# Performance work log

Hardware: AMD Instinct MI355X
Metric: run time of the kernel (lower is better)

The kernel has to match this reference:

```python
import jax, jax.numpy as jnp
import numpy as np
from jax import lax

B, S, H = 2, 512, 2048          # batch, seq, hidden_size
I = 768                          # moe_intermediate_size
E = 64                           # num_experts
K = 8                            # num_experts_per_tok (top_k)


def setup_inputs() -> dict:
    key = jax.random.key(0)
    k1, k2, k3, k4 = jax.random.split(key, 4)
    hidden_states = jax.random.normal(k1, (B, S, H), jnp.float32)
    gate_weight = jax.random.normal(k2, (E, H), jnp.float32) * 0.02
    gate_up_weights = jax.random.normal(k3, (E, H, 2 * I), jnp.float32) * 0.02
    down_weights = jax.random.normal(k4, (E, I, H), jnp.float32) * 0.02
    return {
        "hidden_states": hidden_states,
        "gate_weight": gate_weight,
        "gate_up_weights": gate_up_weights,
        "down_weights": down_weights,
    }


def reference(hidden_states, gate_weight, gate_up_weights, down_weights):
    orig_shape = hidden_states.shape
    x = hidden_states.reshape(-1, H)          # [T, H]
    T = x.shape[0]

    # Router: softmax in fp32, top-k, renormalize (norm_topk_prob=True)
    logits = x @ gate_weight.T                # [T, E]
    probs = jax.nn.softmax(logits.astype(jnp.float32), axis=-1)
    routing_weights, selected_experts = lax.top_k(probs, K)   # [T, K]
    wsum = routing_weights.sum(axis=-1, keepdims=True)
    wsum = jnp.where(wsum == 0, 1.0, wsum)
    routing_weights = (routing_weights / wsum).astype(x.dtype)

    # Dense combine matrix [T, E]: zero weight for unselected experts.
    combine = jnp.zeros((T, E), x.dtype).at[
        jnp.arange(T)[:, None], selected_experts
    ].add(routing_weights)

    # Scan over experts; each step is one batched GEMM over all tokens,
    # masked/weighted by the combine weights (same math as per-token loop).
    def body(acc, ws):
        wgu, wd, we = ws                      # [H,2I], [I,H], [T]
        gu = x @ wgu                          # [T, 2I]
        gate, up = jnp.split(gu, 2, axis=-1)  # [T, I] each
        act = jax.nn.silu(gate) * up          # SwiGLU
        out = act @ wd                        # [T, H]
        return acc + we[:, None] * out, None

    init = jnp.zeros_like(x)
    final, _ = lax.scan(body, init, (gate_up_weights, down_weights, combine.T))
    return final.reshape(orig_shape)
```

## Files before the change

kernel.cpp:

```cpp
#include <hip/hip_runtime.h>
#include <hip/hip_bf16.h>
#include <hip/hip_fp16.h>

typedef unsigned int uint32;
typedef unsigned short u16;

#define TOK 1024
#define HID 2048
#define NEXP 64
#define TOPK 8
#define IMED 768
#define IMED2 1536

typedef __attribute__((ext_vector_type(8))) _Float16 half8;
typedef __attribute__((ext_vector_type(4))) float f32x4;

static __device__ __forceinline__ uint32 pack2(float a, float b) {
  union { _Float16 h[2]; uint32 u; } p;
  p.h[0] = (_Float16)a; p.h[1] = (_Float16)b;
  return p.u;
}
static __device__ __forceinline__ u16 f2h(float a) {
  union { _Float16 h; u16 u; } p;
  p.h = (_Float16)a;
  return p.u;
}

__global__ __launch_bounds__(256) void router_kernel(
    const float* __restrict__ x, const float* __restrict__ gw,
    int* __restrict__ topk_id, float* __restrict__ topk_w,
    u16* __restrict__ xh) {
  int t0 = blockIdx.x << 2;
  __shared__ float part[4][NEXP][5];
  int tid = threadIdx.x;
  int e = tid & 63, p = tid >> 6;
  const float* gwp = gw + (size_t)e * HID + (p << 9);
  const float* xp = x + (size_t)t0 * HID + (p << 9);
  float acc[4] = {0.f, 0.f, 0.f, 0.f};
  for (int i = 0; i < 128; i++) {
    float4 w = ((const float4*)gwp)[i];
    #pragma unroll
    for (int t = 0; t < 4; t++) {
      float4 xv = *(const float4*)(xp + (size_t)t * HID + (i << 2));
      acc[t] += w.x * xv.x + w.y * xv.y + w.z * xv.z + w.w * xv.w;
    }
  }
  #pragma unroll
  for (int t = 0; t < 4; t++) part[p][e][t] = acc[t];
  for (int i = tid; i < 2048; i += 256) {
    int r = i >> 9;
    int c = i & 511;
    float4 v = *(const float4*)(x + (size_t)(t0 + r) * HID + (c << 2));
    uint2 hp;
    hp.x = pack2(v.x, v.y);
    hp.y = pack2(v.z, v.w);
    *(uint2*)(xh + (size_t)(t0 + r) * HID + (c << 2)) = hp;
  }
  __syncthreads();
  int wv = tid >> 6, l = tid & 63;
  int t = t0 + wv;
  float lg = part[0][l][wv] + part[1][l][wv] + part[2][l][wv] + part[3][l][wv];
  float m = lg;
  #pragma unroll
  for (int d = 1; d < 64; d <<= 1) m = fmaxf(m, __shfl_xor(m, d));
  float v = __expf(lg - m);
  float w8[TOPK]; int i8[TOPK]; float wsum = 0.f;
  #pragma unroll
  for (int k = 0; k < TOPK; k++) {
    float bv = v; int bi = l;
    #pragma unroll
    for (int d = 1; d < 64; d <<= 1) {
      float ov = __shfl_xor(bv, d);
      int oi = __shfl_xor(bi, d);
      if (ov > bv || (ov == bv && oi < bi)) { bv = ov; bi = oi; }
    }
    w8[k] = bv; i8[k] = bi; wsum += bv;
    if (l == bi) v = -1.f;
  }
  if (l == 0) {
    float rinv = 1.f / wsum;
    #pragma unroll
    for (int k = 0; k < TOPK; k++) {
      topk_id[t * TOPK + k] = i8[k];
      topk_w[t * TOPK + k] = w8[k] * rinv;
    }
  }
}

__global__ __launch_bounds__(256) void scatter_kernel(
    const int* __restrict__ topk_id, const float* __restrict__ topk_w,
    int* __restrict__ off, int* __restrict__ gcnt,
    int* __restrict__ row_tok, float* __restrict__ row_w,
    int* __restrict__ inv) {
  int e = blockIdx.x;
  __shared__ int lcnt[NEXP];
  __shared__ int sbase;
  __shared__ int scur;
  int tid = threadIdx.x;
  if (tid < NEXP) lcnt[tid] = 0;
  __syncthreads();
  for (int i = tid; i < TOK * TOPK; i += 256) atomicAdd(&lcnt[topk_id[i]], 1);
  __syncthreads();
  if (tid < 64) {
    int c = lcnt[tid];
    int xv = c;
    #pragma unroll
    for (int d = 1; d < 64; d <<= 1) {
      int y = __shfl_up(xv, d);
      if (tid >= d) xv += y;
    }
    if (tid == e) {
      sbase = xv - c;
      off[e] = xv - c;
      gcnt[e] = c;
    }
    if (tid == 0) scur = 0;
  }
  __syncthreads();
  int base = sbase;
  for (int i = tid; i < TOK * TOPK; i += 256) {
    if (topk_id[i] == e) {
      int p = atomicAdd(&scur, 1);
      row_tok[base + p] = i >> 3;
      row_w[base + p] = topk_w[i];
      inv[i] = base + p;
    }
  }
}

__global__ __launch_bounds__(512, 2) void gateup_kernel(
    const u16* __restrict__ xh, const float* __restrict__ Wgu,
    const int* __restrict__ off, const int* __restrict__ cnt,
    const int* __restrict__ row_tok, u16* __restrict__ act) {
  int bid = blockIdx.x;
  int xcd = bid & 7, s2 = bid >> 3;
  int e = xcd + ((s2 & 7) << 3);
  int slab = s2 >> 3;
  int r0 = off[e];
  int ne = cnt[e];
  int c0 = slab * 96;

  __shared__ __align__(16) char AsB[256 * 80];
  __shared__ __align__(16) char BsB[192 * 80];

  int tid = threadIdx.x;
  int lane = tid & 63;
  int wid = tid >> 6;
  int wm = wid >> 1, wn = wid & 1;
  int fr = lane & 15, hi = lane >> 4;

  int arow = tid >> 1, aseg = tid & 1;
  int tok = row_tok[r0 + ((arow < ne) ? arow : 0)];
  const u16* xa = xh + (size_t)tok * HID + (aseg << 4);
  int axr = (arow >> 2) & 3;

  bool bact = tid < 384;
  int cg = tid % 24, h = (tid / 24) & 1, kq = tid / 48;
  int bcol = cg << 2;
  int gc = h ? (IMED + c0 + bcol) : (c0 + bcol);
  const float* wb = Wgu + (size_t)e * ((size_t)HID * IMED2) + (size_t)(kq << 2) * IMED2 + gc;
  int brbase = 96 * h + bcol;

  f32x4 accg[4][3], accu[4][3];
  #pragma unroll
  for (int a = 0; a < 4; a++)
    #pragma unroll
    for (int b = 0; b < 3; b++) { accg[a][b] = (f32x4)0.f; accu[a][b] = (f32x4)0.f; }

  uint4 qa0, qa1;
  float4 w0, w1, w2, w3;
  auto LOADT = [&]() {
    const uint4* p = (const uint4*)xa;
    qa0 = p[0]; qa1 = p[1];
    xa += 32;
    if (bact) {
      w0 = *(const float4*)(wb);
      w1 = *(const float4*)(wb + IMED2);
      w2 = *(const float4*)(wb + 2 * IMED2);
      w3 = *(const float4*)(wb + 3 * IMED2);
    }
    wb += (size_t)32 * IMED2;
  };
  auto STORET = [&]() {
    char* A_ = AsB + arow * 80;
    int g0 = aseg << 1;
    *(uint4*)(A_ + (((g0 + 0) ^ axr) << 4)) = qa0;
    *(uint4*)(A_ + (((g0 + 1) ^ axr) << 4)) = qa1;
    if (bact) {
      float c0v[4] = {w0.x, w0.y, w0.z, w0.w};
      float c1v[4] = {w1.x, w1.y, w1.z, w1.w};
      float c2v[4] = {w2.x, w2.y, w2.z, w2.w};
      float c3v[4] = {w3.x, w3.y, w3.z, w3.w};
      int kg = kq >> 1, kb = (kq & 1) << 3;
      #pragma unroll
      for (int cc = 0; cc < 4; cc++) {
        int br = brbase + cc;
        uint2 pv;
        pv.x = pack2(c0v[cc], c1v[cc]);
        pv.y = pack2(c2v[cc], c3v[cc]);
        *(uint2*)(BsB + br * 80 + (((kg ^ (br >> 2)) & 3) << 4) + kb) = pv;
      }
    }
  };

  const int NK = HID / 32;
  LOADT();
  STORET();
  LOADT();
  __syncthreads();

  for (int t = 0; t < NK; ++t) {
    half8 af[4];
    #pragma unroll
    for (int mi = 0; mi < 4; mi++) {
      int r = (wm << 6) + (mi << 4) + fr;
      af[mi] = *(half8*)(AsB + r * 80 + (((hi ^ (r >> 2)) & 3) << 4));
    }
    #pragma unroll
    for (int ni = 0; ni < 3; ni++) {
      int ng = (wn * 48) + (ni << 4) + fr;
      int nu = ng + 96;
      half8 bg = *(half8*)(BsB + ng * 80 + (((hi ^ (ng >> 2)) & 3) << 4));
      half8 bu = *(half8*)(BsB + nu * 80 + (((hi ^ (nu >> 2)) & 3) << 4));
      #pragma unroll
      for (int mi = 0; mi < 4; mi++) {
        accg[mi][ni] = __builtin_amdgcn_mfma_f32_16x16x32_f16(af[mi], bg, accg[mi][ni], 0, 0, 0);
        accu[mi][ni] = __builtin_amdgcn_mfma_f32_16x16x32_f16(af[mi], bu, accu[mi][ni], 0, 0, 0);
      }
    }
    __syncthreads();
    if (t + 1 < NK) {
      STORET();
      if (t + 2 < NK) LOADT();
      __syncthreads();
    }
  }

  #pragma unroll
  for (int mi = 0; mi < 4; mi++) {
    #pragma unroll
    for (int ni = 0; ni < 3; ni++) {
      int col = c0 + wn * 48 + (ni << 4) + fr;
      #pragma unroll
      for (int r = 0; r < 4; r++) {
        int rr = (wm << 6) + (mi << 4) + (hi << 2) + r;
        if (rr < ne) {
          float g = accg[mi][ni][r];
          float u = accu[mi][ni][r];
          float s = g / (1.f + __expf(-g)) * u;
          act[(size_t)(r0 + rr) * IMED + col] = f2h(s);
        }
      }
    }
  }
}

__global__ __launch_bounds__(512, 2) void down_kernel(
    const u16* __restrict__ act, const float* __restrict__ Wd,
    const int* __restrict__ off, const int* __restrict__ cnt,
    const float* __restrict__ row_w, u16* __restrict__ dscr) {
  int bid = blockIdx.x;
  int xcd = bid & 7, s2 = bid >> 3;
  int e = xcd + ((s2 & 7) << 3);
  int slab = s2 >> 3;
  int r0 = off[e];
  int ne = cnt[e];
  int n0 = slab << 8;

  __shared__ __align__(16) char AsB[256 * 80];
  __shared__ __align__(16) char BsB[256 * 80];

  int tid = threadIdx.x;
  int lane = tid & 63;
  int wid = tid >> 6;
  int wm = wid >> 1, wn = wid & 1;
  int fr = lane & 15, hi = lane >> 4;

  int arow = tid >> 1, aseg = tid & 1;
  const u16* ap = act + (size_t)(r0 + ((arow < ne) ? arow : 0)) * IMED + (aseg << 4);
  int axr = (arow >> 2) & 3;

  int cq = tid & 63, kq = tid >> 6;
  int bcol = cq << 2;
  const float* wb = Wd + (size_t)e * ((size_t)IMED * HID) + (size_t)(kq << 2) * HID + n0 + bcol;

  f32x4 acc[4][8];
  #pragma unroll
  for (int a = 0; a < 4; a++)
    #pragma unroll
    for (int b = 0; b < 8; b++) acc[a][b] = (f32x4)0.f;

  uint4 qa0, qa1;
  float4 w0, w1, w2, w3;
  auto LOADT = [&]() {
    const uint4* p = (const uint4*)ap;
    qa0 = p[0]; qa1 = p[1];
    ap += 32;
    w0 = *(const float4*)(wb);
    w1 = *(const float4*)(wb + HID);
    w2 = *(const float4*)(wb + 2 * HID);
    w3 = *(const float4*)(wb + 3 * HID);
    wb += (size_t)32 * HID;
  };
  auto STORET = [&]() {
    char* A_ = AsB + arow * 80;
    int g0 = aseg << 1;
    *(uint4*)(A_ + (((g0 + 0) ^ axr) << 4)) = qa0;
    *(uint4*)(A_ + (((g0 + 1) ^ axr) << 4)) = qa1;
    float c0v[4] = {w0.x, w0.y, w0.z, w0.w};
    float c1v[4] = {w1.x, w1.y, w1.z, w1.w};
    float c2v[4] = {w2.x, w2.y, w2.z, w2.w};
    float c3v[4] = {w3.x, w3.y, w3.z, w3.w};
    int kg = kq >> 1, kb = (kq & 1) << 3;
    #pragma unroll
    for (int cc = 0; cc < 4; cc++) {
      int br = bcol + cc;
      uint2 pv;
      pv.x = pack2(c0v[cc], c1v[cc]);
      pv.y = pack2(c2v[cc], c3v[cc]);
      *(uint2*)(BsB + br * 80 + (((kg ^ (br >> 2)) & 3) << 4) + kb) = pv;
    }
  };

  const int NK = IMED / 32;
  LOADT();
  STORET();
  LOADT();
  __syncthreads();

  for (int t = 0; t < NK; ++t) {
    half8 af[4];
    #pragma unroll
    for (int mi = 0; mi < 4; mi++) {
      int r = (wm << 6) + (mi << 4) + fr;
      af[mi] = *(half8*)(AsB + r * 80 + (((hi ^ (r >> 2)) & 3) << 4));
    }
    #pragma unroll
    for (int ni = 0; ni < 8; ni++) {
      int n = (wn << 7) + (ni << 4) + fr;
      half8 bf_ = *(half8*)(BsB + n * 80 + (((hi ^ (n >> 2)) & 3) << 4));
      #pragma unroll
      for (int mi = 0; mi < 4; mi++)
        acc[mi][ni] = __builtin_amdgcn_mfma_f32_16x16x32_f16(af[mi], bf_, acc[mi][ni], 0, 0, 0);
    }
    __syncthreads();
    if (t + 1 < NK) {
      STORET();
      if (t + 2 < NK) LOADT();
      __syncthreads();
    }
  }

  #pragma unroll
  for (int mi = 0; mi < 4; mi++) {
    #pragma unroll
    for (int r = 0; r < 4; r++) {
      int rr = (wm << 6) + (mi << 4) + (hi << 2) + r;
      if (rr < ne) {
        float w = row_w[r0 + rr];
        #pragma unroll
        for (int ni = 0; ni < 8; ni++) {
          int col = n0 + (wn << 7) + (ni << 4) + fr;
          dscr[(size_t)(r0 + rr) * HID + col] = f2h(acc[mi][ni][r] * w);
        }
      }
    }
  }
}

__global__ __launch_bounds__(256) void combine_kernel(
    const u16* __restrict__ dscr, const int* __restrict__ inv,
    float* __restrict__ out) {
  int t = blockIdx.x;
  int c0 = threadIdx.x << 3;
  int rows[TOPK];
  #pragma unroll
  for (int k = 0; k < TOPK; k++) rows[k] = inv[t * TOPK + k];
  float s[8] = {0.f, 0.f, 0.f, 0.f, 0.f, 0.f, 0.f, 0.f};
  #pragma unroll
  for (int k = 0; k < TOPK; k++) {
    union { uint4 q; _Float16 h[8]; } u;
    u.q = *(const uint4*)(dscr + (size_t)rows[k] * HID + c0);
    #pragma unroll
    for (int j = 0; j < 8; j++) s[j] += (float)u.h[j];
  }
  float4 o0 = {s[0], s[1], s[2], s[3]};
  float4 o1 = {s[4], s[5], s[6], s[7]};
  *(float4*)(out + (size_t)t * HID + c0) = o0;
  *(float4*)(out + (size_t)t * HID + c0 + 4) = o1;
}

extern "C" void kernel_launch(void* const* d_in, const int* in_sizes, int n_in,
                              void* d_out, int out_size, void* d_ws, size_t ws_size,
                              hipStream_t stream) {
  const float* x = (const float*)d_in[0];
  const float* gw = (const float*)d_in[1];
  const float* wgu = (const float*)d_in[2];
  const float* wd = (const float*)d_in[3];
  float* out = (float*)d_out;
  char* ws = (char*)d_ws;

  int* gcnt = (int*)(ws + 0);
  int* off = (int*)(ws + 512);
  int* topk_id = (int*)(ws + 1024);
  float* topk_w = (float*)(ws + 1024 + 32768);
  int* row_tok = (int*)(ws + 1024 + 65536);
  float* row_w = (float*)(ws + 1024 + 98304);
  u16* act = (u16*)(ws + 135168);
  u16* xh = (u16*)(ws + 135168 + 12582912);
  int* inv = (int*)(ws + 135168 + 12582912 + 4194304);
  u16* dscr = (u16*)(ws + 135168 + 12582912 + 4194304 + 32768);

  router_kernel<<<TOK / 4, 256, 0, stream>>>(x, gw, topk_id, topk_w, xh);
  scatter_kernel<<<NEXP, 256, 0, stream>>>(topk_id, topk_w, off, gcnt, row_tok, row_w, inv);
  gateup_kernel<<<512, 512, 0, stream>>>(xh, wgu, off, gcnt, row_tok, act);
  down_kernel<<<512, 512, 0, stream>>>(act, wd, off, gcnt, row_w, dscr);
  combine_kernel<<<TOK, 256, 0, stream>>>(dscr, inv, out);
}
```

Measured before the change: 364.7 us.

## Fuse combine into down GEMM via atomic adds and use nontemporal weight loads

Removes the separate combine kernel and the fp16 scratch buffer. The down-projection kernel now scales each row by its routing weight and atomically adds it straight into the fp32 output, which is zeroed with a memset first. Weight loads in both GEMM kernels switch to nontemporal loads so the streamed weights pollute the cache less. The trade-off is contention from about 16M float atomics and an order of accumulation that is no longer deterministic.

```diff
diff --git a/kernel.cpp b/kernel.cpp
--- a/kernel.cpp
+++ b/kernel.cpp
@@ -14,6 +14,7 @@
 
 typedef __attribute__((ext_vector_type(8))) _Float16 half8;
 typedef __attribute__((ext_vector_type(4))) float f32x4;
+typedef __attribute__((ext_vector_type(4))) float nf4;
 
 static __device__ __forceinline__ uint32 pack2(float a, float b) {
   union { _Float16 h[2]; uint32 u; } p;
@@ -90,8 +91,7 @@
 __global__ __launch_bounds__(256) void scatter_kernel(
     const int* __restrict__ topk_id, const float* __restrict__ topk_w,
     int* __restrict__ off, int* __restrict__ gcnt,
-    int* __restrict__ row_tok, float* __restrict__ row_w,
-    int* __restrict__ inv) {
+    int* __restrict__ row_tok, float* __restrict__ row_w) {
   int e = blockIdx.x;
   __shared__ int lcnt[NEXP];
   __shared__ int sbase;
@@ -123,7 +123,6 @@
       int p = atomicAdd(&scur, 1);
       row_tok[base + p] = i >> 3;
       row_w[base + p] = topk_w[i];
-      inv[i] = base + p;
     }
   }
 }
@@ -168,16 +167,16 @@
     for (int b = 0; b < 3; b++) { accg[a][b] = (f32x4)0.f; accu[a][b] = (f32x4)0.f; }
 
   uint4 qa0, qa1;
-  float4 w0, w1, w2, w3;
+  nf4 w0, w1, w2, w3;
   auto LOADT = [&]() {
     const uint4* p = (const uint4*)xa;
     qa0 = p[0]; qa1 = p[1];
     xa += 32;
     if (bact) {
-      w0 = *(const float4*)(wb);
-      w1 = *(const float4*)(wb + IMED2);
-      w2 = *(const float4*)(wb + 2 * IMED2);
-      w3 = *(const float4*)(wb + 3 * IMED2);
+      w0 = __builtin_nontemporal_load((const nf4*)(wb));
+      w1 = __builtin_nontemporal_load((const nf4*)(wb + IMED2));
+      w2 = __builtin_nontemporal_load((const nf4*)(wb + 2 * IMED2));
+      w3 = __builtin_nontemporal_load((const nf4*)(wb + 3 * IMED2));
     }
     wb += (size_t)32 * IMED2;
   };
@@ -258,7 +257,8 @@
 __global__ __launch_bounds__(512, 2) void down_kernel(
     const u16* __restrict__ act, const float* __restrict__ Wd,
     const int* __restrict__ off, const int* __restrict__ cnt,
-    const float* __restrict__ row_w, u16* __restrict__ dscr) {
+    const int* __restrict__ row_tok, const float* __restrict__ row_w,
+    float* __restrict__ out) {
   int bid = blockIdx.x;
   int xcd = bid & 7, s2 = bid >> 3;
   int e = xcd + ((s2 & 7) << 3);
@@ -291,15 +291,15 @@
     for (int b = 0; b < 8; b++) acc[a][b] = (f32x4)0.f;
 
   uint4 qa0, qa1;
-  float4 w0, w1, w2, w3;
+  nf4 w0, w1, w2, w3;
   auto LOADT = [&]() {
     const uint4* p = (const uint4*)ap;
     qa0 = p[0]; qa1 = p[1];
     ap += 32;
-    w0 = *(const float4*)(wb);
-    w1 = *(const float4*)(wb + HID);
-    w2 = *(const float4*)(wb + 2 * HID);
-    w3 = *(const float4*)(wb + 3 * HID);
+    w0 = __builtin_nontemporal_load((const nf4*)(wb));
+    w1 = __builtin_nontemporal_load((const nf4*)(wb + HID));
+    w2 = __builtin_nontemporal_load((const nf4*)(wb + 2 * HID));
+    w3 = __builtin_nontemporal_load((const nf4*)(wb + 3 * HID));
     wb += (size_t)32 * HID;
   };
   auto STORET = [&]() {
@@ -358,36 +358,15 @@
       int rr = (wm << 6) + (mi << 4) + (hi << 2) + r;
       if (rr < ne) {
         float w = row_w[r0 + rr];
+        int t = row_tok[r0 + rr];
         #pragma unroll
         for (int ni = 0; ni < 8; ni++) {
           int col = n0 + (wn << 7) + (ni << 4) + fr;
-          dscr[(size_t)(r0 + rr) * HID + col] = f2h(acc[mi][ni][r] * w);
+          unsafeAtomicAdd(&out[(size_t)t * HID + col], acc[mi][ni][r] * w);
         }
       }
     }
   }
-}
-
-__global__ __launch_bounds__(256) void combine_kernel(
-    const u16* __restrict__ dscr, const int* __restrict__ inv,
-    float* __restrict__ out) {
-  int t = blockIdx.x;
-  int c0 = threadIdx.x << 3;
-  int rows[TOPK];
-  #pragma unroll
-  for (int k = 0; k < TOPK; k++) rows[k] = inv[t * TOPK + k];
-  float s[8] = {0.f, 0.f, 0.f, 0.f, 0.f, 0.f, 0.f, 0.f};
-  #pragma unroll
-  for (int k = 0; k < TOPK; k++) {
-    union { uint4 q; _Float16 h[8]; } u;
-    u.q = *(const uint4*)(dscr + (size_t)rows[k] * HID + c0);
-    #pragma unroll
-    for (int j = 0; j < 8; j++) s[j] += (float)u.h[j];
-  }
-  float4 o0 = {s[0], s[1], s[2], s[3]};
-  float4 o1 = {s[4], s[5], s[6], s[7]};
-  *(float4*)(out + (size_t)t * HID + c0) = o0;
-  *(float4*)(out + (size_t)t * HID + c0 + 4) = o1;
 }
 
 extern "C" void kernel_launch(void* const* d_in, const int* in_sizes, int n_in,
@@ -408,12 +387,10 @@
   float* row_w = (float*)(ws + 1024 + 98304);
   u16* act = (u16*)(ws + 135168);
   u16* xh = (u16*)(ws + 135168 + 12582912);
-  int* inv = (int*)(ws + 135168 + 12582912 + 4194304);
-  u16* dscr = (u16*)(ws + 135168 + 12582912 + 4194304 + 32768);
 
   router_kernel<<<TOK / 4, 256, 0, stream>>>(x, gw, topk_id, topk_w, xh);
-  scatter_kernel<<<NEXP, 256, 0, stream>>>(topk_id, topk_w, off, gcnt, row_tok, row_w, inv);
+  scatter_kernel<<<NEXP, 256, 0, stream>>>(topk_id, topk_w, off, gcnt, row_tok, row_w);
+  (void)hipMemsetAsync(out, 0, (size_t)TOK * HID * sizeof(float), stream);
   gateup_kernel<<<512, 512, 0, stream>>>(xh, wgu, off, gcnt, row_tok, act);
-  down_kernel<<<512, 512, 0, stream>>>(act, wd, off, gcnt, row_w, dscr);
-  combine_kernel<<<TOK, 256, 0, stream>>>(dscr, inv, out);
-}
+  down_kernel<<<512, 512, 0, stream>>>(act, wd, off, gcnt, row_tok, row_w, out);
+}
```

After: 370.4 us. Within noise of the previous version (+1.6%).
